# Optimization experiments

Hardware: AMD Instinct MI355X
Metric: run time of the kernel (lower is better)

## Reference

```python
import jax, jax.numpy as jnp
import numpy as np

EPS = 1e-07


def _splat_one(inp, idx4, w4, n):
    # inp: [C1, N] weighted features for one batch element
    # idx4: [4, N] int32 flat target indices (clipped)
    # w4:  [4, N] bilinear weights (zeroed where out of bounds)
    out = jnp.zeros((inp.shape[0], n), dtype=inp.dtype)
    for k in range(4):
        out = out.at[:, idx4[k]].add(inp * w4[k])
    return out


def _softsplat(x, flow, metric):
    B, C, H, W = x.shape
    N = H * W
    m = jnp.exp(metric)                      # [B,1,H,W]
    inp = jnp.concatenate([x * m, m], axis=1)  # [B,C+1,H,W]

    gy, gx = jnp.meshgrid(jnp.arange(H, dtype=x.dtype),
                          jnp.arange(W, dtype=x.dtype), indexing='ij')
    tx = gx[None] + flow[:, 0]               # [B,H,W] target x
    ty = gy[None] + flow[:, 1]               # [B,H,W] target y

    x0f = jnp.floor(tx)
    y0f = jnp.floor(ty)
    x0 = x0f.astype(jnp.int32)
    y0 = y0f.astype(jnp.int32)
    x1 = x0 + 1
    y1 = y0 + 1

    fx = tx - x0f                            # frac parts
    fy = ty - y0f
    # bilinear weights for (x0,y0),(x1,y0),(x0,y1),(x1,y1)
    w = jnp.stack([(1 - fx) * (1 - fy),
                   fx * (1 - fy),
                   (1 - fx) * fy,
                   fx * fy], axis=1)          # [B,4,H,W]
    xs = jnp.stack([x0, x1, x0, x1], axis=1)  # [B,4,H,W]
    ys = jnp.stack([y0, y0, y1, y1], axis=1)

    valid = (xs >= 0) & (xs < W) & (ys >= 0) & (ys < H)
    w = jnp.where(valid, w, 0.0).reshape(B, 4, N)
    idx = (jnp.clip(ys, 0, H - 1) * W + jnp.clip(xs, 0, W - 1)).reshape(B, 4, N)

    inp_flat = inp.reshape(B, C + 1, N)
    out = jax.vmap(lambda i, ix, ww: _splat_one(i, ix, ww, N))(inp_flat, idx, w)
    out = out.reshape(B, C + 1, H, W)
    return out[:, :-1] / (out[:, -1:] + EPS)


def setup_inputs() -> dict:
    key = jax.random.key(0)
    k1, k2, k3 = jax.random.split(key, 3)
    x = jax.random.normal(k1, (8, 64, 256, 448), dtype=jnp.float32)
    flow = jax.random.normal(k2, (8, 2, 256, 448), dtype=jnp.float32)
    metric = jax.random.normal(k3, (8, 1, 256, 448), dtype=jnp.float32)
    return {"x": x, "flow": flow, "metric": metric}


def reference(x, flow, metric):
    return _softsplat(x, flow, metric)
```

## Files before the change

### kernel.cpp

```cpp
#include <hip/hip_runtime.h>

#define EPS 1e-7f

constexpr int B = 8, C = 64, H = 256, W = 448;
constexpr int N = H * W;
constexpr int P = B * N;

constexpr int TS  = 16;
constexpr int NT  = 256;
constexpr int RW  = 8;
constexpr int WIN = 32;
constexpr int NW  = WIN * WIN;
constexpr int K   = 19;
constexpr int CHB = 8;
constexpr int NCHUNK = C / CHB;
constexpr float FMAX = 7.0f;
constexpr int TX = W / TS, TY = H / TS;
constexpr int TILES = B * TX * TY;
constexpr int NXCD = 8;

constexpr int L_FXY = 0, L_EM = 2112, L_PK = 3136;
constexpr int LDS_WORDS = 8192;

typedef __fp16 h2_t __attribute__((ext_vector_type(2)));
static __device__ __forceinline__ unsigned pk2(float a, float b) {
    h2_t h = __builtin_amdgcn_cvt_pkrtz(a, b);
    return __builtin_bit_cast(unsigned, h);
}
static __device__ __forceinline__ float2 up2(unsigned u) {
    h2_t h = __builtin_bit_cast(h2_t, u);
    return make_float2((float)h.x, (float)h.y);
}

__device__ int g_flag;

__global__ void zero_flag_k() { g_flag = 0; }

__global__ __launch_bounds__(256) void flag_scan(const float* __restrict__ flow)
{
    int t = blockIdx.x * blockDim.x + threadIdx.x;
    if (t >= P) return;
    int b = t / N, p = t - b * N;
    float fdx = flow[(size_t)(b * 2 + 0) * N + p];
    float fdy = flow[(size_t)(b * 2 + 1) * N + p];
    if (fabsf(fdx) > FMAX || fabsf(fdy) > FMAX) atomicAdd(&g_flag, 1);
}

#define STAGE_LOAD(gg)                                                        \
    {                                                                         \
        const int cbase = (gg) * CHB;                                         \
        const int row = tid >> 3;                                             \
        const int sc0 = (tid & 7) * 4;                                        \
        const int sh = ty0 - RW + row;                                        \
        const int sc = tx0 - RW + sc0;                                        \
        const bool v = (sh >= 0) & (sh < H) & (sc >= 0) & (sc < W);           \
        const float* bp = xb + (sh * W + sc);                                 \
        _Pragma("unroll")                                                     \
        for (int ch = 0; ch < CHB; ++ch)                                      \
            fr[ch] = v ? *(const float4*)(bp + (size_t)(cbase + ch) * N)      \
                       : make_float4(0.f, 0.f, 0.f, 0.f);                     \
    }

#define STAGE_WRITE(bufsel)                                                   \
    {                                                                         \
        char* base = (char*)lds + (bufsel) * 16384;                           \
        _Pragma("unroll")                                                     \
        for (int k = 0; k < 4; ++k) {                                         \
            const unsigned pos = 4u * (unsigned)tid + (unsigned)k;            \
            const unsigned blk = pos ^ ((pos >> 3) & 7u);                     \
            uint4 wv;                                                         \
            wv.x = pk2(((const float*)&fr[0])[k], ((const float*)&fr[1])[k]); \
            wv.y = pk2(((const float*)&fr[2])[k], ((const float*)&fr[3])[k]); \
            wv.z = pk2(((const float*)&fr[4])[k], ((const float*)&fr[5])[k]); \
            wv.w = pk2(((const float*)&fr[6])[k], ((const float*)&fr[7])[k]); \
            *(uint4*)(base + blk * 16) = wv;                                  \
        }                                                                     \
    }

__global__ __launch_bounds__(NT) void softsplat_fused(
    const float* __restrict__ x,
    const float* __restrict__ flow,
    const float* __restrict__ metric,
    float* __restrict__ out,
    float* __restrict__ den)
{
    __shared__ float lds[LDS_WORDS];
    float*    s_fxy = lds + L_FXY;
    float*    s_em  = lds + L_EM;
    unsigned* s_pk  = (unsigned*)(lds + L_PK);

    int bid = blockIdx.x;
    bid = (bid % NXCD) * (TILES / NXCD) + bid / NXCD;

    const int b   = bid / (TX * TY);
    const int tp  = bid % (TX * TY);
    const int ty0 = (tp / TX) * TS;
    const int tx0 = (tp % TX) * TS;
    const int tid = threadIdx.x;

    const float* fxg = flow + (size_t)(b * 2 + 0) * N;
    const float* fyg = flow + (size_t)(b * 2 + 1) * N;
    const float* mg  = metric + (size_t)b * N;

    float mymax = 0.f;
    for (int i = tid; i < NW; i += NT) {
        const int wy = i >> 5, wx = i & 31;
        const int sh = ty0 - RW + wy, sw = tx0 - RW + wx;
        float fdx = 1.0e9f, fdy = 0.f, em = 0.f;
        if (sh >= 0 && sh < H && sw >= 0 && sw < W) {
            const int sp = sh * W + sw;
            const float a = fxg[sp], bb = fyg[sp];
            if (fabsf(a) <= FMAX && fabsf(bb) <= FMAX) {
                fdx = a; fdy = bb; em = __expf(mg[sp]);
                mymax = fmaxf(mymax, fmaxf(fabsf(a), fabsf(bb)));
            }
        }
        const int fi = wy * 33 + wx;
        s_fxy[2 * fi] = fdx; s_fxy[2 * fi + 1] = fdy; s_em[i] = em;
    }
    #pragma unroll
    for (int m = 1; m < 64; m <<= 1) mymax = fmaxf(mymax, __shfl_xor(mymax, m));
    if ((tid & 63) == 0) lds[L_PK + (tid >> 6)] = mymax;
    __syncthreads();
    const float M = fmaxf(fmaxf(lds[L_PK + 0], lds[L_PK + 1]),
                          fmaxf(lds[L_PK + 2], lds[L_PK + 3]));
    const int Rdyn = min(RW, (int)M + 1);
    __syncthreads();

    const int qxl = tid & (TS - 1), qyl = tid >> 4;
    const int qx = tx0 + qxl, qy = ty0 + qyl;
    const int q  = qy * W + qx;

    int cnt = 0;
    float dacc = 0.f;
    for (int dy = -Rdyn; dy <= Rdyn; ++dy) {
        const int lrow = qyl + RW + dy;
        for (int dx = -Rdyn; dx <= Rdyn; ++dx) {
            const int lcol = qxl + RW + dx;
            const int fi = lrow * 33 + lcol;
            const float fdx = s_fxy[2 * fi];
            const float tx = (float)(qx + dx) + fdx;
            const float x0f = floorf(tx);
            const int ddx = qx - (int)x0f;
            if ((unsigned)ddx > 1u) continue;
            const float fdy = s_fxy[2 * fi + 1];
            const float tyy = (float)(qy + dy) + fdy;
            const float y0f = floorf(tyy);
            const int ddy = qy - (int)y0f;
            if ((unsigned)ddy > 1u) continue;
            const float fxf = tx - x0f, fyf = tyy - y0f;
            const float wxf = ddx ? fxf : 1.f - fxf;
            const float wyf = ddy ? fyf : 1.f - fyf;
            const float w = wxf * wyf * s_em[lrow * WIN + lcol];
            if (cnt < K) {
                const unsigned pos = (unsigned)(lrow * WIN + lcol);
                s_pk[cnt * NT + tid] = (__float_as_uint(w) & 0xFFFFFC00u) | pos;
            }
            cnt++;
            dacc += w;
        }
    }
    for (int j = cnt; j < K; ++j)
        s_pk[j * NT + tid] = (unsigned)((qyl + RW) * WIN + (qxl + RW));

    int km = cnt;
    #pragma unroll
    for (int m = 1; m < 64; m <<= 1) km = max(km, __shfl_xor(km, m));
    const int kwave = min(K, __builtin_amdgcn_readfirstlane(km));

    const int flag = g_flag;
    const float rn = (flag == 0) ? 1.f / (dacc + EPS) : 1.f;

    const float* xb = x + (size_t)b * C * N;
    float* ob = out + (size_t)b * C * N + q;
    den[(size_t)b * N + q] = dacc;

    unsigned rsp[K]; float rw_[K];
    #pragma unroll
    for (int j = 0; j < K; ++j) {
        const unsigned pk = s_pk[j * NT + tid];
        const unsigned pos = pk & 0x3FFu;
        rsp[j] = (pos ^ ((pos >> 3) & 7u)) << 4;
        rw_[j] = __uint_as_float(pk & 0xFFFFFC00u);
    }

    const bool ovf = (cnt > K);
    if (ovf) {
        for (int c = 0; c < C; ++c) {
            const float* xp = xb + (size_t)c * N;
            float a = 0.f;
            for (int dy = -Rdyn; dy <= Rdyn; ++dy) {
                const int lrow = qyl + RW + dy;
                for (int dx = -Rdyn; dx <= Rdyn; ++dx) {
                    const int lcol = qxl + RW + dx;
                    const int fi = lrow * 33 + lcol;
                    const float fdx = s_fxy[2 * fi];
                    const float tx = (float)(qx + dx) + fdx;
                    const float x0f = floorf(tx);
                    const int ddx = qx - (int)x0f;
                    if ((unsigned)ddx > 1u) continue;
                    const float fdy = s_fxy[2 * fi + 1];
                    const float tyy = (float)(qy + dy) + fdy;
                    const float y0f = floorf(tyy);
                    const int ddy = qy - (int)y0f;
                    if ((unsigned)ddy > 1u) continue;
                    const float fxf = tx - x0f, fyf = tyy - y0f;
                    const float wxf = ddx ? fxf : 1.f - fxf;
                    const float wyf = ddy ? fyf : 1.f - fyf;
                    a = fmaf(wxf * wyf * s_em[lrow * WIN + lcol],
                             xp[(qy + dy) * W + (qx + dx)], a);
                }
            }
            ob[(size_t)c * N] = a * rn;
        }
    }
    __syncthreads();

    float4 fr[CHB];
    STAGE_LOAD(0)
    STAGE_WRITE(0)
    __syncthreads();
    for (int g = 0; g < NCHUNK; ++g) {
        const char* bc = (const char*)lds + (g & 1) * 16384;
        if (g + 1 < NCHUNK) STAGE_LOAD(g + 1)
        float a0 = 0.f, a1 = 0.f, a2 = 0.f, a3 = 0.f;
        float a4 = 0.f, a5 = 0.f, a6 = 0.f, a7 = 0.f;
        #pragma unroll
        for (int j = 0; j < K; ++j) {
            if (j >= kwave) break;
            const uint4 v = *(const uint4*)(bc + rsp[j]);
            const float wj = rw_[j];
            float2 p;
            p = up2(v.x); a0 = fmaf(wj, p.x, a0); a1 = fmaf(wj, p.y, a1);
            p = up2(v.y); a2 = fmaf(wj, p.x, a2); a3 = fmaf(wj, p.y, a3);
            p = up2(v.z); a4 = fmaf(wj, p.x, a4); a5 = fmaf(wj, p.y, a5);
            p = up2(v.w); a6 = fmaf(wj, p.x, a6); a7 = fmaf(wj, p.y, a7);
        }
        if (!ovf) {
            ob[(size_t)(g * CHB + 0) * N] = a0 * rn;
            ob[(size_t)(g * CHB + 1) * N] = a1 * rn;
            ob[(size_t)(g * CHB + 2) * N] = a2 * rn;
            ob[(size_t)(g * CHB + 3) * N] = a3 * rn;
            ob[(size_t)(g * CHB + 4) * N] = a4 * rn;
            ob[(size_t)(g * CHB + 5) * N] = a5 * rn;
            ob[(size_t)(g * CHB + 6) * N] = a6 * rn;
            ob[(size_t)(g * CHB + 7) * N] = a7 * rn;
        }
        if (g + 1 < NCHUNK) STAGE_WRITE((g & 1) ^ 1)
        __syncthreads();
    }
}

__global__ __launch_bounds__(256) void softsplat_outlier(
    const float* __restrict__ x,
    const float* __restrict__ flow,
    const float* __restrict__ metric,
    float* __restrict__ out,
    float* __restrict__ den)
{
    int t = blockIdx.x * blockDim.x + threadIdx.x;
    if (t >= P) return;
    int b = t / N;
    int p = t - b * N;
    float fdx = flow[(size_t)(b * 2 + 0) * N + p];
    float fdy = flow[(size_t)(b * 2 + 1) * N + p];
    if (fabsf(fdx) <= FMAX && fabsf(fdy) <= FMAX) return;

    int h = p / W, w = p - h * W;
    float m = __expf(metric[(size_t)b * N + p]);
    float tx = (float)w + fdx, ty = (float)h + fdy;
    float x0f = floorf(tx), y0f = floorf(ty);
    int x0 = (int)x0f, y0 = (int)y0f, x1 = x0 + 1, y1 = y0 + 1;
    float fx = tx - x0f, fy = ty - y0f;
    float w00 = (1.f - fx) * (1.f - fy), w10 = fx * (1.f - fy);
    float w01 = (1.f - fx) * fy,         w11 = fx * fy;
    bool vx0 = (x0 >= 0) && (x0 < W), vx1 = (x1 >= 0) && (x1 < W);
    bool vy0 = (y0 >= 0) && (y0 < H), vy1 = (y1 >= 0) && (y1 < H);
    int cx0 = min(max(x0, 0), W - 1), cx1 = min(max(x1, 0), W - 1);
    int cy0 = min(max(y0, 0), H - 1), cy1 = min(max(y1, 0), H - 1);
    int i00 = cy0 * W + cx0, i10 = cy0 * W + cx1;
    int i01 = cy1 * W + cx0, i11 = cy1 * W + cx1;
    w00 = (vx0 && vy0) ? w00 * m : 0.f;
    w10 = (vx1 && vy0) ? w10 * m : 0.f;
    w01 = (vx0 && vy1) ? w01 * m : 0.f;
    w11 = (vx1 && vy1) ? w11 * m : 0.f;

    float* denb = den + (size_t)b * N;
    if (w00 != 0.f) atomicAdd(denb + i00, w00);
    if (w10 != 0.f) atomicAdd(denb + i10, w10);
    if (w01 != 0.f) atomicAdd(denb + i01, w01);
    if (w11 != 0.f) atomicAdd(denb + i11, w11);

    const float* xb = x + (size_t)b * C * N + p;
    float* ob = out + (size_t)b * C * N;
    for (int c = 0; c < C; ++c) {
        float v = xb[(size_t)c * N];
        float* o = ob + (size_t)c * N;
        if (w00 != 0.f) atomicAdd(o + i00, v * w00);
        if (w10 != 0.f) atomicAdd(o + i10, v * w10);
        if (w01 != 0.f) atomicAdd(o + i01, v * w01);
        if (w11 != 0.f) atomicAdd(o + i11, v * w11);
    }
}

__global__ __launch_bounds__(256) void softsplat_norm(
    float* __restrict__ out, const float* __restrict__ den)
{
    if (g_flag == 0) return;
    size_t t = (size_t)blockIdx.x * blockDim.x + threadIdx.x;
    size_t e = t * 4;
    if (e >= (size_t)B * C * N) return;
    size_t b = e / ((size_t)C * N);
    size_t p = (e - b * (size_t)C * N) % N;

    float4 o = *reinterpret_cast<float4*>(out + e);
    const float4 d = *reinterpret_cast<const float4*>(den + b * N + p);
    o.x = o.x / (d.x + EPS);
    o.y = o.y / (d.y + EPS);
    o.z = o.z / (d.z + EPS);
    o.w = o.w / (d.w + EPS);
    *reinterpret_cast<float4*>(out + e) = o;
}

extern "C" void kernel_launch(void* const* d_in, const int* in_sizes, int n_in,
                              void* d_out, int out_size, void* d_ws, size_t ws_size,
                              hipStream_t stream) {
    const float* x      = (const float*)d_in[0];
    const float* flow   = (const float*)d_in[1];
    const float* metric = (const float*)d_in[2];
    float* out = (float*)d_out;
    float* den = (float*)d_ws;

    zero_flag_k<<<1, 1, 0, stream>>>();
    flag_scan<<<(P + 255) / 256, 256, 0, stream>>>(flow);

    softsplat_fused<<<TILES, NT, 0, stream>>>(x, flow, metric, out, den);

    softsplat_outlier<<<(P + 255) / 256, 256, 0, stream>>>(x, flow, metric, out, den);

    size_t nvec4 = (size_t)B * C * N / 4;
    softsplat_norm<<<(int)((nvec4 + 255) / 256), 256, 0, stream>>>(out, den);
}
```

Measured before the change: 251.4 us.

## Precompute integer splat targets per source pixel and fold normalization into weights

Each window pixel's floored target coordinates are computed once, packed into a single 32-bit word in LDS, and stored along with its fractional offsets in separate arrays. The gather loop then tests whether a source hits the query pixel with integer subtracts instead of per-neighbour float adds and floors. The normalization factor is folded into the cached weights, which removes the per-output multiply. K drops from 19 to 15, cutting register use but sending more pixels down the slow overflow path.

```diff
diff --git a/kernel.cpp b/kernel.cpp
--- a/kernel.cpp
+++ b/kernel.cpp
@@ -11,7 +11,8 @@
 constexpr int RW  = 8;
 constexpr int WIN = 32;
 constexpr int NW  = WIN * WIN;
-constexpr int K   = 19;
+constexpr int TGS = 40;
+constexpr int K   = 15;
 constexpr int CHB = 8;
 constexpr int NCHUNK = C / CHB;
 constexpr float FMAX = 7.0f;
@@ -19,7 +20,7 @@
 constexpr int TILES = B * TX * TY;
 constexpr int NXCD = 8;
 
-constexpr int L_FXY = 0, L_EM = 2112, L_PK = 3136;
+constexpr int L_TGT = 0, L_FX = 1280, L_FY = 2304, L_EM = 3328, L_PK = 4352;
 constexpr int LDS_WORDS = 8192;
 
 typedef __fp16 h2_t __attribute__((ext_vector_type(2)));
@@ -85,7 +86,9 @@
     float* __restrict__ den)
 {
     __shared__ float lds[LDS_WORDS];
-    float*    s_fxy = lds + L_FXY;
+    unsigned* s_tgt = (unsigned*)(lds + L_TGT);
+    float*    s_fx  = lds + L_FX;
+    float*    s_fy  = lds + L_FY;
     float*    s_em  = lds + L_EM;
     unsigned* s_pk  = (unsigned*)(lds + L_PK);
 
@@ -106,17 +109,22 @@
     for (int i = tid; i < NW; i += NT) {
         const int wy = i >> 5, wx = i & 31;
         const int sh = ty0 - RW + wy, sw = tx0 - RW + wx;
-        float fdx = 1.0e9f, fdy = 0.f, em = 0.f;
+        unsigned t = 0xFFFFFFFFu;
         if (sh >= 0 && sh < H && sw >= 0 && sw < W) {
             const int sp = sh * W + sw;
             const float a = fxg[sp], bb = fyg[sp];
             if (fabsf(a) <= FMAX && fabsf(bb) <= FMAX) {
-                fdx = a; fdy = bb; em = __expf(mg[sp]);
+                const float xf = floorf(a), yf = floorf(bb);
+                const int tx0g = sw + (int)xf + 16;
+                const int ty0g = sh + (int)yf + 16;
+                t = ((unsigned)ty0g << 16) | (unsigned)tx0g;
+                s_fx[i] = a - xf;
+                s_fy[i] = bb - yf;
+                s_em[i] = __expf(mg[sp]);
                 mymax = fmaxf(mymax, fmaxf(fabsf(a), fabsf(bb)));
             }
         }
-        const int fi = wy * 33 + wx;
-        s_fxy[2 * fi] = fdx; s_fxy[2 * fi + 1] = fdy; s_em[i] = em;
+        s_tgt[wy * TGS + wx] = t;
     }
     #pragma unroll
     for (int m = 1; m < 64; m <<= 1) mymax = fmaxf(mymax, __shfl_xor(mymax, m));
@@ -130,32 +138,25 @@
     const int qxl = tid & (TS - 1), qyl = tid >> 4;
     const int qx = tx0 + qxl, qy = ty0 + qyl;
     const int q  = qy * W + qx;
+    const unsigned qx16 = (unsigned)(qx + 16), qy16 = (unsigned)(qy + 16);
 
     int cnt = 0;
     float dacc = 0.f;
     for (int dy = -Rdyn; dy <= Rdyn; ++dy) {
         const int lrow = qyl + RW + dy;
+        const int trow = lrow * TGS + (qxl + RW);
         for (int dx = -Rdyn; dx <= Rdyn; ++dx) {
-            const int lcol = qxl + RW + dx;
-            const int fi = lrow * 33 + lcol;
-            const float fdx = s_fxy[2 * fi];
-            const float tx = (float)(qx + dx) + fdx;
-            const float x0f = floorf(tx);
-            const int ddx = qx - (int)x0f;
-            if ((unsigned)ddx > 1u) continue;
-            const float fdy = s_fxy[2 * fi + 1];
-            const float tyy = (float)(qy + dy) + fdy;
-            const float y0f = floorf(tyy);
-            const int ddy = qy - (int)y0f;
-            if ((unsigned)ddy > 1u) continue;
-            const float fxf = tx - x0f, fyf = tyy - y0f;
-            const float wxf = ddx ? fxf : 1.f - fxf;
-            const float wyf = ddy ? fyf : 1.f - fyf;
-            const float w = wxf * wyf * s_em[lrow * WIN + lcol];
-            if (cnt < K) {
-                const unsigned pos = (unsigned)(lrow * WIN + lcol);
-                s_pk[cnt * NT + tid] = (__float_as_uint(w) & 0xFFFFFC00u) | pos;
-            }
+            const unsigned t = s_tgt[trow + dx];
+            const unsigned du = qx16 - (t & 0xFFFFu);
+            const unsigned dv = qy16 - (t >> 16);
+            if (max(du, dv) > 1u) continue;
+            const int fi = lrow * WIN + (qxl + RW + dx);
+            const float fxf = s_fx[fi], fyf = s_fy[fi];
+            const float wxf = du ? fxf : 1.f - fxf;
+            const float wyf = dv ? fyf : 1.f - fyf;
+            const float w = wxf * wyf * s_em[fi];
+            if (cnt < K)
+                s_pk[cnt * NT + tid] = (__float_as_uint(w) & 0xFFFFFC00u) | (unsigned)fi;
             cnt++;
             dacc += w;
         }
@@ -181,7 +182,7 @@
         const unsigned pk = s_pk[j * NT + tid];
         const unsigned pos = pk & 0x3FFu;
         rsp[j] = (pos ^ ((pos >> 3) & 7u)) << 4;
-        rw_[j] = __uint_as_float(pk & 0xFFFFFC00u);
+        rw_[j] = __uint_as_float(pk & 0xFFFFFC00u) * rn;
     }
 
     const bool ovf = (cnt > K);
@@ -191,24 +192,17 @@
             float a = 0.f;
             for (int dy = -Rdyn; dy <= Rdyn; ++dy) {
                 const int lrow = qyl + RW + dy;
+                const int trow = lrow * TGS + (qxl + RW);
                 for (int dx = -Rdyn; dx <= Rdyn; ++dx) {
-                    const int lcol = qxl + RW + dx;
-                    const int fi = lrow * 33 + lcol;
-                    const float fdx = s_fxy[2 * fi];
-                    const float tx = (float)(qx + dx) + fdx;
-                    const float x0f = floorf(tx);
-                    const int ddx = qx - (int)x0f;
-                    if ((unsigned)ddx > 1u) continue;
-                    const float fdy = s_fxy[2 * fi + 1];
-                    const float tyy = (float)(qy + dy) + fdy;
-                    const float y0f = floorf(tyy);
-                    const int ddy = qy - (int)y0f;
-                    if ((unsigned)ddy > 1u) continue;
-                    const float fxf = tx - x0f, fyf = tyy - y0f;
-                    const float wxf = ddx ? fxf : 1.f - fxf;
-                    const float wyf = ddy ? fyf : 1.f - fyf;
-                    a = fmaf(wxf * wyf * s_em[lrow * WIN + lcol],
-                             xp[(qy + dy) * W + (qx + dx)], a);
+                    const unsigned t = s_tgt[trow + dx];
+                    const unsigned du = qx16 - (t & 0xFFFFu);
+                    const unsigned dv = qy16 - (t >> 16);
+                    if (max(du, dv) > 1u) continue;
+                    const int fi = lrow * WIN + (qxl + RW + dx);
+                    const float fxf = s_fx[fi], fyf = s_fy[fi];
+                    const float wxf = du ? fxf : 1.f - fxf;
+                    const float wyf = dv ? fyf : 1.f - fyf;
+                    a = fmaf(wxf * wyf * s_em[fi], xp[(qy + dy) * W + (qx + dx)], a);
                 }
             }
             ob[(size_t)c * N] = a * rn;
@@ -237,14 +231,14 @@
             p = up2(v.w); a6 = fmaf(wj, p.x, a6); a7 = fmaf(wj, p.y, a7);
         }
         if (!ovf) {
-            ob[(size_t)(g * CHB + 0) * N] = a0 * rn;
-            ob[(size_t)(g * CHB + 1) * N] = a1 * rn;
-            ob[(size_t)(g * CHB + 2) * N] = a2 * rn;
-            ob[(size_t)(g * CHB + 3) * N] = a3 * rn;
-            ob[(size_t)(g * CHB + 4) * N] = a4 * rn;
-            ob[(size_t)(g * CHB + 5) * N] = a5 * rn;
-            ob[(size_t)(g * CHB + 6) * N] = a6 * rn;
-            ob[(size_t)(g * CHB + 7) * N] = a7 * rn;
+            ob[(size_t)(g * CHB + 0) * N] = a0;
+            ob[(size_t)(g * CHB + 1) * N] = a1;
+            ob[(size_t)(g * CHB + 2) * N] = a2;
+            ob[(size_t)(g * CHB + 3) * N] = a3;
+            ob[(size_t)(g * CHB + 4) * N] = a4;
+            ob[(size_t)(g * CHB + 5) * N] = a5;
+            ob[(size_t)(g * CHB + 6) * N] = a6;
+            ob[(size_t)(g * CHB + 7) * N] = a7;
         }
         if (g + 1 < NCHUNK) STAGE_WRITE((g & 1) ^ 1)
         __syncthreads();
```

Result: faster. 238.7 us (-5.1%).
